# Optimization experiments

Hardware: AMD Instinct MI355X
Metric: run time of the kernel (lower is better)

The kernel has to match this reference:

```python
import jax, jax.numpy as jnp
import numpy as np

FEATURE_DIM = 1024
HIDDEN_DIM = FEATURE_DIM // 4  # MetaNet default: max(input_dim//4, output_dim) = 256
NUM_TASKS = 8
BATCH = 8192


def setup_inputs() -> dict:
    key = jax.random.key(0)
    ks = jax.random.split(key, 8)
    features = jax.random.normal(ks[0], (BATCH, FEATURE_DIM), dtype=jnp.float32)
    # meta_net: Linear(D->H) -> ReLU -> Linear(H->K). Scaled so coefficients straddle the threshold.
    W1 = jax.random.normal(ks[1], (HIDDEN_DIM, FEATURE_DIM), dtype=jnp.float32) * 0.02
    b1 = jax.random.normal(ks[2], (HIDDEN_DIM,), dtype=jnp.float32) * 0.01
    W2 = jax.random.normal(ks[3], (NUM_TASKS, HIDDEN_DIM), dtype=jnp.float32) * 0.1
    b2 = jax.random.normal(ks[4], (NUM_TASKS,), dtype=jnp.float32) * 0.05
    # per-task feature transforms, init randn * 0.01 as in the module
    task_mats = jax.random.normal(ks[5], (NUM_TASKS, FEATURE_DIM, FEATURE_DIM), dtype=jnp.float32) * 0.01
    # projection initialized to identity (nn.init.eye_)
    proj_W = jnp.eye(FEATURE_DIM, dtype=jnp.float32)
    base_threshold = jnp.array([0.05], dtype=jnp.float32)
    beta = jnp.array([1.0], dtype=jnp.float32)
    return {"features": features, "W1": W1, "b1": b1, "W2": W2, "b2": b2,
            "task_mats": task_mats, "proj_W": proj_W,
            "base_threshold": base_threshold, "beta": beta}


def reference(features, W1, b1, W2, b2, task_mats, proj_W, base_threshold, beta):
    # --- meta_net forward: coefficients [B, K] ---
    h = features @ W1.T + b1                    # [B, H]
    relu_h = jnp.maximum(h, 0.0)
    coeffs = relu_h @ W2.T + b2                 # [B, K]

    # --- gradient-based uncertainty: ||d coeff_k / d features_b||_2 ---
    # Jacobian of the 2-layer MLP: J[b,k,d] = sum_h W2[k,h] * relu'(h[b,h]) * W1[h,d]
    mask = (h > 0).astype(features.dtype)       # [B, H]
    J = jnp.einsum('kh,bh,hd->bkd', W2, mask, W1)   # [B, K, D]
    unc = jnp.sqrt(jnp.sum(J * J, axis=-1))     # [B, K]
    mx = jnp.max(unc)
    unc = jnp.where(mx > 0, unc / mx, unc)
    # torch computes this on detached features with create_graph=False -> non-differentiable
    unc = jax.lax.stop_gradient(unc)

    # --- adaptive gating ---
    base = jax.nn.softplus(base_threshold)                  # [1]
    thresholds = base * (1.0 + jax.nn.relu(beta) * unc)     # [B, K]
    gated = jnp.where(jnp.abs(coeffs) < thresholds, 0.0, coeffs)  # [B, K]

    # --- sequential weighted task-vector combination (blockwise=False) ---
    x = features                                # [B, D]
    for j in range(task_mats.shape[0]):         # small fixed K, structurally sequential
        x = x + gated[:, j:j + 1] * (x @ task_mats[j])
    return x @ proj_W.T                         # [B, D]
```

## Files before the change

### kernel.cpp

```cpp
#include <hip/hip_runtime.h>


typedef float  f32x4  __attribute__((ext_vector_type(4)));
typedef __bf16 bf16x8 __attribute__((ext_vector_type(8)));
typedef _Float16 f16x8 __attribute__((ext_vector_type(8)));
typedef _Float16 f16x4 __attribute__((ext_vector_type(4)));

__device__ __forceinline__ unsigned short f2bf(float x) {
  return __builtin_bit_cast(unsigned short, (__bf16)x);
}
__device__ __forceinline__ float bf2f(unsigned short u) {
  return (float)__builtin_bit_cast(__bf16, u);
}
__device__ __forceinline__ void ldsload16(void* lds, const void* g) {
  __builtin_amdgcn_global_load_lds(
      (const __attribute__((address_space(1))) void*)g,
      (__attribute__((address_space(3))) void*)lds, 16, 0, 0);
}


__global__ __launch_bounds__(256) void k_initsplit(const float* __restrict__ F,
                                                   _Float16* __restrict__ hi,
                                                   _Float16* __restrict__ lo,
                                                   float* __restrict__ xout,
                                                   unsigned short* __restrict__ xhA,
                                                   unsigned short* __restrict__ xhB) {
  size_t i = (size_t)blockIdx.x * 256 + threadIdx.x;
  float4 f = *(const float4*)&F[i * 4];
  _Float16 h0 = (_Float16)f.x, h1 = (_Float16)f.y, h2 = (_Float16)f.z, h3 = (_Float16)f.w;
  *(f16x4*)&hi[i * 4] = (f16x4){h0, h1, h2, h3};
  *(f16x4*)&lo[i * 4] = (f16x4){(_Float16)((f.x - (float)h0) * 2048.0f),
                                (_Float16)((f.y - (float)h1) * 2048.0f),
                                (_Float16)((f.z - (float)h2) * 2048.0f),
                                (_Float16)((f.w - (float)h3) * 2048.0f)};
  *(float4*)&xout[i * 4] = f;
  ushort4 u;
  u.x = f2bf(f.x); u.y = f2bf(f.y); u.z = f2bf(f.z); u.w = f2bf(f.w);
  *(ushort4*)&xhA[i * 4] = u;
  *(ushort4*)&xhB[i * 4] = u;
}

__global__ __launch_bounds__(256) void k_split(const float* __restrict__ src,
                                               _Float16* __restrict__ hi,
                                               _Float16* __restrict__ lo) {
  size_t i = (size_t)blockIdx.x * 256 + threadIdx.x;
  float4 f = *(const float4*)&src[i * 4];
  _Float16 h0 = (_Float16)f.x, h1 = (_Float16)f.y, h2 = (_Float16)f.z, h3 = (_Float16)f.w;
  *(f16x4*)&hi[i * 4] = (f16x4){h0, h1, h2, h3};
  *(f16x4*)&lo[i * 4] = (f16x4){(_Float16)((f.x - (float)h0) * 2048.0f),
                                (_Float16)((f.y - (float)h1) * 2048.0f),
                                (_Float16)((f.z - (float)h2) * 2048.0f),
                                (_Float16)((f.w - (float)h3) * 2048.0f)};
}

__global__ __launch_bounds__(256) void k_gram(const float* __restrict__ W1,
                                              float* __restrict__ G) {
  __shared__ float Wa[16][33], Wb[16][33];
  int t = threadIdx.x, ti = t & 15, tj = t >> 4;
  int bi = blockIdx.x, bj = blockIdx.y;
  float acc = 0.f;
  for (int kc = 0; kc < 1024; kc += 32) {
    __syncthreads();
    for (int e = t; e < 512; e += 256) {
      int r = e >> 5, k = e & 31;
      Wa[r][k] = W1[(size_t)(bi * 16 + r) * 1024 + kc + k];
      Wb[r][k] = W1[(size_t)(bj * 16 + r) * 1024 + kc + k];
    }
    __syncthreads();
#pragma unroll
    for (int k = 0; k < 32; k++) acc += Wa[ti][k] * Wb[tj][k];
  }
  G[(size_t)(bi * 16 + ti) * 256 + bj * 16 + tj] = acc;
}

__global__ __launch_bounds__(256) void k_prepA(const float* __restrict__ W2,
                                               const float* __restrict__ G,
                                               unsigned short* __restrict__ Bk,
                                               unsigned int* __restrict__ mx,
                                               int* __restrict__ cnt,
                                               int* __restrict__ cnt2,
                                               unsigned int* __restrict__ flag) {
  int k = blockIdx.x >> 8, hr = blockIdx.x & 255, t = threadIdx.x;
  if (blockIdx.x == 0) {
    if (t == 0) { *mx = 0u; *flag = 1u; }
    if (t < 8) { cnt[t] = 0; cnt2[t] = 0; }
  }
  float v = W2[k * 256 + hr] * W2[k * 256 + t] * G[(size_t)hr * 256 + t];
  float hi = bf2f(f2bf(v));
  float lo = v - hi;
  unsigned short* row = &Bk[((size_t)k * 256 + hr) * 512];
  row[t] = f2bf(hi);
  row[256 + t] = f2bf(lo);
}

__global__ __launch_bounds__(256) void k_maskcoef(const float* __restrict__ h,
                                                  const float* __restrict__ W2,
                                                  const float* __restrict__ b2,
                                                  unsigned short* __restrict__ Mb,
                                                  unsigned int* __restrict__ Mbits,
                                                  float* __restrict__ coeffs) {
  __shared__ float W2s[2048];
  __shared__ unsigned sw[4][8];
  int t = threadIdx.x;
  for (int e = t; e < 2048; e += 256) W2s[e] = W2[e];
  int w = t >> 6, l = t & 63;
  int row = blockIdx.x * 4 + w;
  float4 hv = *(const float4*)&h[(size_t)row * 256 + l * 4];
  ushort4 mv;
  mv.x = hv.x > 0.f ? 0x3F80 : 0; mv.y = hv.y > 0.f ? 0x3F80 : 0;
  mv.z = hv.z > 0.f ? 0x3F80 : 0; mv.w = hv.w > 0.f ? 0x3F80 : 0;
  *(ushort4*)&Mb[(size_t)row * 256 + l * 4] = mv;
  unsigned nib = (hv.x > 0.f ? 1u : 0u) | (hv.y > 0.f ? 2u : 0u) |
                 (hv.z > 0.f ? 4u : 0u) | (hv.w > 0.f ? 8u : 0u);
  if (l < 8) sw[w][l] = 0u;
  __syncthreads();
  atomicOr(&sw[w][l >> 3], nib << ((l & 7) * 4));
  __syncthreads();
  if (l < 8) Mbits[row * 8 + l] = sw[w][l];
  float r0 = fmaxf(hv.x, 0.f), r1 = fmaxf(hv.y, 0.f);
  float r2 = fmaxf(hv.z, 0.f), r3 = fmaxf(hv.w, 0.f);
#pragma unroll
  for (int k = 0; k < 8; k++) {
    const float* wr = &W2s[k * 256 + l * 4];
    float p = r0 * wr[0] + r1 * wr[1] + r2 * wr[2] + r3 * wr[3];
    p += __shfl_xor(p, 1);  p += __shfl_xor(p, 2);  p += __shfl_xor(p, 4);
    p += __shfl_xor(p, 8);  p += __shfl_xor(p, 16); p += __shfl_xor(p, 32);
    if (l == 0) coeffs[row * 8 + k] = p + b2[k];
  }
}

__global__ __launch_bounds__(256) void k_max(const float* __restrict__ unc2,
                                             unsigned int* __restrict__ mx) {
  int i = blockIdx.x * 256 + threadIdx.x;
  float v = 0.f;
  for (; i < 65536; i += 64 * 256) v = fmaxf(v, unc2[i]);
#pragma unroll
  for (int d = 1; d < 64; d <<= 1) v = fmaxf(v, __shfl_xor(v, d));
  __shared__ float sm[4];
  if ((threadIdx.x & 63) == 0) sm[threadIdx.x >> 6] = v;
  __syncthreads();
  if (threadIdx.x == 0) {
    v = fmaxf(fmaxf(sm[0], sm[1]), fmaxf(sm[2], sm[3]));
    atomicMax(mx, __float_as_uint(v));
  }
}

__global__ __launch_bounds__(256) void k_gateidx(const float* __restrict__ coeffs,
                                                 const float* __restrict__ unc2,
                                                 const unsigned int* __restrict__ mxb,
                                                 const float* __restrict__ btp,
                                                 const float* __restrict__ betap,
                                                 unsigned short* __restrict__ rowidx,
                                                 float* __restrict__ gcomp,
                                                 int* __restrict__ cnt,
                                                 unsigned short* __restrict__ rowidx2,
                                                 int* __restrict__ cnt2) {
  __shared__ int lc[8], base[8], lc2[8], base2[8];
  __shared__ float sgv[256];
  int t = threadIdx.x;
  if (t < 8) { lc[t] = 0; lc2[t] = 0; }
  __syncthreads();
  int i = blockIdx.x * 256 + t;
  float c = coeffs[i];
  float u2 = fmaxf(unc2[i], 0.f);
  float un = sqrtf(u2);
  float m = sqrtf(__uint_as_float(*mxb));
  float u = (m > 0.f) ? un / m : un;
  float base_t = (float)log1p(exp((double)btp[0]));
  float br = fmaxf(betap[0], 0.f);
  float thr = base_t * (1.0f + br * u);
  float gv = (fabsf(c) < thr) ? 0.f : c;
  sgv[t] = gv;
  int jj = i & 7, row = i >> 3, slot = -1;
  if (gv != 0.f) slot = atomicAdd(&lc[jj], 1);
  __syncthreads();
  int slot2 = -1;
  if (jj >= 1 && gv == 0.f && sgv[t - 1] != 0.f) slot2 = atomicAdd(&lc2[jj], 1);
  __syncthreads();
  if (t < 8) {
    base[t]  = lc[t]  ? atomicAdd(&cnt[t],  lc[t])  : 0;
    base2[t] = lc2[t] ? atomicAdd(&cnt2[t], lc2[t]) : 0;
  }
  __syncthreads();
  if (slot >= 0) {
    int pos = base[jj] + slot;
    rowidx[jj * 8192 + pos] = (unsigned short)row;
    gcomp[jj * 8192 + pos] = gv;
  }
  if (slot2 >= 0)
    rowidx2[jj * 8192 + base2[jj] + slot2] = (unsigned short)row;
}

__global__ __launch_bounds__(256) void k_prepT(const float* __restrict__ TM,
                                               unsigned short* __restrict__ Tb) {
  __shared__ float Ls[64][65];
  int bid = blockIdx.x;
  int jj = bid >> 8, kt = (bid >> 4) & 15, nt = bid & 15;
  int t = threadIdx.x;
  int r = t >> 2, c0 = (t & 3) * 16;
  const float* src = TM + (size_t)jj * 1048576 + (size_t)(kt * 64 + r) * 1024 + nt * 64 + c0;
  float4 v0 = *(const float4*)&src[0];
  float4 v1 = *(const float4*)&src[4];
  float4 v2 = *(const float4*)&src[8];
  float4 v3 = *(const float4*)&src[12];
  float tmp[16] = {v0.x, v0.y, v0.z, v0.w, v1.x, v1.y, v1.z, v1.w,
                   v2.x, v2.y, v2.z, v2.w, v3.x, v3.y, v3.z, v3.w};
#pragma unroll
  for (int i = 0; i < 16; i++) Ls[r][c0 + i] = tmp[i];
  __syncthreads();
  int nr = t >> 2, kc = (t & 3) * 16;
  union { unsigned short s[16]; uint4 v[2]; } p;
#pragma unroll
  for (int i = 0; i < 16; i++) p.s[i] = f2bf(Ls[kc + i][nr]);
  unsigned short* dst = Tb + (size_t)jj * 1048576 + (size_t)(nt * 64 + nr) * 1024 + kt * 64 + kc;
  *(uint4*)&dst[0] = p.v[0];
  *(uint4*)&dst[8] = p.v[1];
}

__global__ __launch_bounds__(256) void k_prepP2(const float* __restrict__ P,
                                                unsigned short* __restrict__ Pb,
                                                unsigned int* __restrict__ flag) {
  size_t i = (size_t)blockIdx.x * 256 + threadIdx.x;
  float4 f = *(const float4*)&P[i * 4];
  ushort4 u;
  u.x = f2bf(f.x); u.y = f2bf(f.y); u.z = f2bf(f.z); u.w = f2bf(f.w);
  *(ushort4*)&Pb[i * 4] = u;
  size_t e = i * 4;
  bool bad = false;
#pragma unroll
  for (int s = 0; s < 4; s++) {
    size_t ee = e + s;
    float exp = ((ee >> 10) == (ee & 1023)) ? 1.0f : 0.0f;
    float got = (s == 0) ? f.x : (s == 1) ? f.y : (s == 2) ? f.z : f.w;
    if (got != exp) bad = true;
  }
  if (bad) atomicAnd(flag, 0u);
}


__global__ __launch_bounds__(256) void k_gemm_h2(const _Float16* __restrict__ Fhi,
                                                 const _Float16* __restrict__ Flo,
                                                 const _Float16* __restrict__ W1h,
                                                 const _Float16* __restrict__ W1l,
                                                 const float* __restrict__ b1,
                                                 float* __restrict__ hout) {
  __shared__ __attribute__((aligned(16))) _Float16 Ah[64 * 32];
  __shared__ __attribute__((aligned(16))) _Float16 Al[64 * 32];
  __shared__ __attribute__((aligned(16))) _Float16 Bh[64 * 32];
  __shared__ __attribute__((aligned(16))) _Float16 Bl[64 * 32];
  int t = threadIdx.x, w = t >> 6, l = t & 63, q = l >> 4, li = l & 15;
  int wm = w >> 1, wn = w & 1;
  int ib = blockIdx.x, jb = blockIdx.y;
  f32x4 acc0[2][2] = {}, acc1[2][2] = {};
  int srow = t >> 2, sg = (((t & 3) - (srow >> 1)) & 3) * 8;
  for (int k0 = 0; k0 < 1024; k0 += 32) {
    __syncthreads();
    size_t ao = (size_t)(ib * 64 + srow) * 1024 + k0 + sg;
    size_t bo = (size_t)(jb * 64 + srow) * 1024 + k0 + sg;
    ldsload16((void*)(Ah + (w * 64) * 8), Fhi + ao);
    ldsload16((void*)(Al + (w * 64) * 8), Flo + ao);
    ldsload16((void*)(Bh + (w * 64) * 8), W1h + bo);
    ldsload16((void*)(Bl + (w * 64) * 8), W1l + bo);
    __syncthreads();
    f16x8 ah[2], al[2], bh[2], bl[2];
#pragma unroll
    for (int mt = 0; mt < 2; mt++) {
      int r = wm * 32 + mt * 16 + li;
      int c = ((q + (r >> 1)) & 3) * 8;
      ah[mt] = *(const f16x8*)&Ah[r * 32 + c];
      al[mt] = *(const f16x8*)&Al[r * 32 + c];
    }
#pragma unroll
    for (int nt = 0; nt < 2; nt++) {
      int rr = wn * 32 + nt * 16 + li;
      int c = ((q + (rr >> 1)) & 3) * 8;
      bh[nt] = *(const f16x8*)&Bh[rr * 32 + c];
      bl[nt] = *(const f16x8*)&Bl[rr * 32 + c];
    }
#pragma unroll
    for (int mt = 0; mt < 2; mt++)
#pragma unroll
      for (int nt = 0; nt < 2; nt++) {
        acc0[mt][nt] = __builtin_amdgcn_mfma_f32_16x16x32_f16(ah[mt], bh[nt], acc0[mt][nt], 0, 0, 0);
        acc1[mt][nt] = __builtin_amdgcn_mfma_f32_16x16x32_f16(ah[mt], bl[nt], acc1[mt][nt], 0, 0, 0);
        acc1[mt][nt] = __builtin_amdgcn_mfma_f32_16x16x32_f16(al[mt], bh[nt], acc1[mt][nt], 0, 0, 0);
      }
  }
  const float sc = 1.0f / 2048.0f;
#pragma unroll
  for (int mt = 0; mt < 2; mt++) {
    int grow = ib * 64 + wm * 32 + mt * 16 + q * 4;
#pragma unroll
    for (int nt = 0; nt < 2; nt++) {
      int gcol = jb * 64 + wn * 32 + nt * 16 + li;
      float bb = b1[gcol];
#pragma unroll
      for (int r = 0; r < 4; r++)
        hout[(size_t)(grow + r) * 256 + gcol] = acc0[mt][nt][r] + acc1[mt][nt][r] * sc + bb;
    }
  }
}

__global__ __launch_bounds__(512) void k_gemm_unc2(const unsigned short* __restrict__ Mb,
                                                   const unsigned short* __restrict__ BkAll,
                                                   const unsigned int* __restrict__ Mbits,
                                                   float* __restrict__ unc2) {
  __shared__ __attribute__((aligned(16))) unsigned short As[128 * 32];
  __shared__ __attribute__((aligned(16))) unsigned short Bs[256 * 32];
  __shared__ float Red[128][4];
  int t = threadIdx.x, w = t >> 6, l = t & 63, q = l >> 4, li = l & 15;
  int wm = w >> 2, wn = w & 3;
  int rb = blockIdx.x, kidx = blockIdx.y;
  const unsigned short* Bk = BkAll + (size_t)kidx * 256 * 512;
  f32x4 acc[4][4] = {};
  for (int k0 = 0; k0 < 512; k0 += 32) {
    __syncthreads();
    {
      int row = t >> 2, g = (((t & 3) - (row >> 1)) & 3) * 8;
      ldsload16((void*)(As + (size_t)(w * 64) * 8),
                Mb + (size_t)(rb * 128 + row) * 256 + (k0 & 255) + g);
    }
#pragma unroll
    for (int i = 0; i < 2; i++) {
      int idx = i * 512 + t, row = idx >> 2, g = (((idx & 3) - (row >> 1)) & 3) * 8;
      ldsload16((void*)(Bs + (size_t)(i * 512 + w * 64) * 8),
                Bk + (size_t)row * 512 + k0 + g);
    }
    __syncthreads();
    bf16x8 av[4], bv[4];
#pragma unroll
    for (int mt = 0; mt < 4; mt++) {
      int r = wm * 64 + mt * 16 + li;
      av[mt] = *(const bf16x8*)&As[r * 32 + ((q + (r >> 1)) & 3) * 8];
    }
#pragma unroll
    for (int nt = 0; nt < 4; nt++) {
      int rc = wn * 64 + nt * 16 + li;
      bv[nt] = *(const bf16x8*)&Bs[rc * 32 + ((q + (rc >> 1)) & 3) * 8];
    }
#pragma unroll
    for (int mt = 0; mt < 4; mt++)
#pragma unroll
      for (int nt = 0; nt < 4; nt++)
        acc[mt][nt] = __builtin_amdgcn_mfma_f32_16x16x32_bf16(av[mt], bv[nt], acc[mt][nt], 0, 0, 0);
  }
#pragma unroll
  for (int mt = 0; mt < 4; mt++) {
#pragma unroll
    for (int r = 0; r < 4; r++) {
      int rl = wm * 64 + mt * 16 + q * 4 + r;
      int grow = rb * 128 + rl;
      unsigned m0 = Mbits[(size_t)grow * 8 + wn * 2];
      unsigned m1 = Mbits[(size_t)grow * 8 + wn * 2 + 1];
      float p = 0.f;
#pragma unroll
      for (int nt = 0; nt < 4; nt++) {
        unsigned mword = (nt < 2) ? m0 : m1;
        int sh = (nt & 1) * 16 + li;
        if ((mword >> sh) & 1u) p += acc[mt][nt][r];
      }
      p += __shfl_xor(p, 1); p += __shfl_xor(p, 2);
      p += __shfl_xor(p, 4); p += __shfl_xor(p, 8);
      if (li == 0) Red[rl][wn] = p;
    }
  }
  __syncthreads();
  if (t < 128)
    unc2[(size_t)(rb * 128 + t) * 8 + kidx] =
        Red[t][0] + Red[t][1] + Red[t][2] + Red[t][3];
}

__global__ __launch_bounds__(1024) void k_chain8(const unsigned short* __restrict__ cur,
                                                 unsigned short* __restrict__ nxt,
                                                 const unsigned short* __restrict__ Tb,
                                                 const unsigned short* __restrict__ rowidx,
                                                 const int* __restrict__ cnt,
                                                 const unsigned short* __restrict__ rowidx2,
                                                 const int* __restrict__ cnt2,
                                                 const float* __restrict__ gcomp,
                                                 float* __restrict__ xout, int j) {
  int Mj = min(max(cnt[j], 0), 8192);
  __shared__ __attribute__((aligned(16))) unsigned short As[64 * 512];
  __shared__ __attribute__((aligned(16))) unsigned short Bs[64 * 512];
  int t = threadIdx.x, w = t >> 6, l = t & 63, q = l >> 4, li = l & 15;
  int wm = w >> 2, wn = w & 3;
  int bx = blockIdx.x, jb = blockIdx.y;
  int bid = jb * 16 + bx;
  const unsigned short* ridx = rowidx + j * 8192;
  {
    int M2 = min(max(cnt2[j], 0), 8192);
    for (int cm2 = bid; cm2 < M2; cm2 += 256) {
      int row = rowidx2[j * 8192 + cm2] & 8191;
      if (t < 128)
        *(uint4*)&nxt[(size_t)row * 1024 + t * 8] =
            *(const uint4*)&cur[(size_t)row * 1024 + t * 8];
    }
  }
  for (int ib = bx; ib * 64 < Mj; ib += 16) {
    f32x4 acc = {};
#pragma unroll 1
    for (int half = 0; half < 2; half++) {
      __syncthreads();
#pragma unroll
      for (int i = 0; i < 4; i++) {
        int slot = i * 1024 + t;
        int r = slot >> 6, kcs = slot & 63;
        int kcg = kcs ^ (r & 7);
        int cm = ib * 64 + r;
        int grow = ridx[cm < Mj ? cm : Mj - 1] & 8191;
        ldsload16((void*)(As + (size_t)(i * 1024 + w * 64) * 8),
                  cur + (size_t)grow * 1024 + half * 512 + kcg * 8);
      }
#pragma unroll
      for (int i = 0; i < 4; i++) {
        int slot = i * 1024 + t;
        int n = slot >> 6, kcs = slot & 63;
        int kcg = kcs ^ (n & 7);
        ldsload16((void*)(Bs + (size_t)(i * 1024 + w * 64) * 8),
                  Tb + (size_t)(jb * 64 + n) * 1024 + half * 512 + kcg * 8);
      }
      __syncthreads();
#pragma unroll
      for (int s = 0; s < 16; s++) {
        int r = wm * 16 + li;
        bf16x8 av = *(const bf16x8*)&As[((size_t)r * 64 + ((s * 4 + q) ^ (r & 7))) * 8];
        int n = wn * 16 + li;
        bf16x8 bv = *(const bf16x8*)&Bs[((size_t)n * 64 + ((s * 4 + q) ^ (n & 7))) * 8];
        acc = __builtin_amdgcn_mfma_f32_16x16x32_bf16(av, bv, acc, 0, 0, 0);
      }
    }
#pragma unroll
    for (int r = 0; r < 4; r++) {
      int cm = ib * 64 + wm * 16 + q * 4 + r;
      if (cm >= Mj) continue;
      int grow = ridx[cm] & 8191;
      float g = gcomp[j * 8192 + cm];
      size_t off = (size_t)grow * 1024 + jb * 64 + wn * 16 + li;
      float xv = fmaf(g, acc[r], xout[off]);
      xout[off] = xv;
      nxt[off] = f2bf(xv);
    }
  }
}

__global__ __launch_bounds__(256) void k_proj3(const unsigned short* __restrict__ xcur,
                                               const unsigned short* __restrict__ Pb,
                                               float* __restrict__ out,
                                               const unsigned int* __restrict__ flag) {
  if (*flag) return;
  __shared__ __attribute__((aligned(16))) unsigned short As[128 * 32];
  __shared__ __attribute__((aligned(16))) unsigned short Bs[128 * 32];
  int t = threadIdx.x, w = t >> 6, l = t & 63, q = l >> 4, li = l & 15;
  int wm = w >> 1, wn = w & 1;
  int ib = blockIdx.x, jb = blockIdx.y;
  f32x4 acc[4][4] = {};
  for (int k0 = 0; k0 < 1024; k0 += 32) {
    __syncthreads();
    const unsigned short* ga = xcur + (size_t)(ib * 128) * 1024 + k0;
    const unsigned short* gb = Pb + (size_t)(jb * 128) * 1024 + k0;
#pragma unroll
    for (int i = 0; i < 2; i++) {
      int idx = i * 256 + t, row = idx >> 2, kc = (idx & 3) * 8;
      ldsload16((void*)(As + (i * 256 + w * 64) * 8), ga + (size_t)row * 1024 + kc);
      ldsload16((void*)(Bs + (i * 256 + w * 64) * 8), gb + (size_t)row * 1024 + kc);
    }
    __syncthreads();
    bf16x8 av[4], bv[4];
#pragma unroll
    for (int mt = 0; mt < 4; mt++)
      av[mt] = *(const bf16x8*)&As[(wm * 64 + mt * 16 + li) * 32 + q * 8];
#pragma unroll
    for (int nt = 0; nt < 4; nt++)
      bv[nt] = *(const bf16x8*)&Bs[(wn * 64 + nt * 16 + li) * 32 + q * 8];
#pragma unroll
    for (int mt = 0; mt < 4; mt++)
#pragma unroll
      for (int nt = 0; nt < 4; nt++)
        acc[mt][nt] = __builtin_amdgcn_mfma_f32_16x16x32_bf16(av[mt], bv[nt], acc[mt][nt], 0, 0, 0);
  }
#pragma unroll
  for (int mt = 0; mt < 4; mt++) {
    int grow = ib * 128 + wm * 64 + mt * 16 + q * 4;
#pragma unroll
    for (int nt = 0; nt < 4; nt++) {
      int gcol = jb * 128 + wn * 64 + nt * 16 + li;
#pragma unroll
      for (int r = 0; r < 4; r++)
        out[(size_t)(grow + r) * 1024 + gcol] = acc[mt][nt][r];
    }
  }
}


extern "C" void kernel_launch(void* const* d_in, const int* in_sizes, int n_in,
                              void* d_out, int out_size, void* d_ws, size_t ws_size,
                              hipStream_t stream) {
  const float* F    = (const float*)d_in[0];
  const float* W1   = (const float*)d_in[1];
  const float* b1   = (const float*)d_in[2];
  const float* W2   = (const float*)d_in[3];
  const float* b2   = (const float*)d_in[4];
  const float* TM   = (const float*)d_in[5];
  const float* PW   = (const float*)d_in[6];
  const float* bt   = (const float*)d_in[7];
  const float* beta = (const float*)d_in[8];

  char* w = (char*)d_ws;
  float*          hbuf   = (float*)         (w + 0);
  unsigned short* Mb     = (unsigned short*)(w + 8388608);
  unsigned int*   Mbits  = (unsigned int*)  (w + 12582912);
  float*          coeffs = (float*)         (w + 12845056);
  float*          unc2   = (float*)         (w + 13107200);
  float*          G      = (float*)         (w + 13369344);
  unsigned short* Bk     = (unsigned short*)(w + 13631488);
  _Float16*       W1h    = (_Float16*)      (w + 15728640);
  _Float16*       W1l    = (_Float16*)      (w + 16252928);
  unsigned short* Tb     = (unsigned short*)(w + 0);
  char*           buf0   =                  (w + 16777216);
  char*           buf1   =                  (w + 33554432);
  unsigned int*   mx     = (unsigned int*)  (w + 50331648);
  int*            cnt    = (int*)           (w + 50331652);
  int*            cnt2   = (int*)           (w + 50331684);
  unsigned int*   flag   = (unsigned int*)  (w + 50331716);
  unsigned short* rowidx = (unsigned short*)(w + 50332160);
  unsigned short* rowidx2= (unsigned short*)(w + 50463232);
  float*          gcomp  = (float*)         (w + 50594304);
  unsigned short* xhA    = (unsigned short*)(w + 50856448);
  unsigned short* xhB    = (unsigned short*)(w + 67633664);
  float* xout = (float*)d_out;

  k_initsplit<<<8192, 256, 0, stream>>>(F, (_Float16*)buf0, (_Float16*)buf1, xout, xhA, xhB);
  k_split<<<256, 256, 0, stream>>>(W1, W1h, W1l);
  k_gram<<<dim3(16, 16), 256, 0, stream>>>(W1, G);
  k_gemm_h2<<<dim3(128, 4), 256, 0, stream>>>((const _Float16*)buf0, (const _Float16*)buf1,
                                              W1h, W1l, b1, hbuf);
  k_maskcoef<<<2048, 256, 0, stream>>>(hbuf, W2, b2, Mb, Mbits, coeffs);
  k_prepA<<<2048, 256, 0, stream>>>(W2, G, Bk, mx, cnt, cnt2, flag);
  k_gemm_unc2<<<dim3(64, 8), 512, 0, stream>>>(Mb, Bk, Mbits, unc2);
  k_max<<<64, 256, 0, stream>>>(unc2, mx);
  k_gateidx<<<256, 256, 0, stream>>>(coeffs, unc2, mx, bt, beta,
                                     rowidx, gcomp, cnt, rowidx2, cnt2);

  k_prepT<<<2048, 256, 0, stream>>>(TM, Tb);
  for (int j = 0; j < 8; j++) {
    const unsigned short* cur = (j & 1) ? xhB : xhA;
    unsigned short*       nxt = (j & 1) ? xhA : xhB;
    k_chain8<<<dim3(16, 16), 1024, 0, stream>>>(cur, nxt, Tb + (size_t)j * 1048576,
                                                rowidx, cnt, rowidx2, cnt2,
                                                gcomp, xout, j);
  }

  unsigned short* Pb = (unsigned short*)buf1;
  k_prepP2<<<1024, 256, 0, stream>>>(PW, Pb, flag);
  k_proj3<<<dim3(64, 8), 256, 0, stream>>>(xhA, Pb, xout, flag);
}
```

Baseline: 352.8 us.

## Fuse prep kernels, split features inside GEMM, and fold max into uncertainty GEMM

Drops the separate fp16 hi/lo split of the feature matrix. The h GEMM now loads fp32 features into LDS through an XOR-swizzled layout and splits them into hi/lo in registers. W1 split and Gram computation merge into one launch, and the projection conversion merges with the task-matrix prep. The max reduction moves into the uncertainty GEMM epilogue via atomicMax, removing several launches and the 64 MB of hi/lo feature traffic, at the cost of extra conversion ALU work and twice the LDS load bytes per GEMM tile.

```diff
diff --git a/kernel.cpp b/kernel.cpp
--- a/kernel.cpp
+++ b/kernel.cpp
@@ -19,20 +19,12 @@
 }
 
 
-__global__ __launch_bounds__(256) void k_initsplit(const float* __restrict__ F,
-                                                   _Float16* __restrict__ hi,
-                                                   _Float16* __restrict__ lo,
-                                                   float* __restrict__ xout,
-                                                   unsigned short* __restrict__ xhA,
-                                                   unsigned short* __restrict__ xhB) {
+__global__ __launch_bounds__(256) void k_initsplit2(const float* __restrict__ F,
+                                                    float* __restrict__ xout,
+                                                    unsigned short* __restrict__ xhA,
+                                                    unsigned short* __restrict__ xhB) {
   size_t i = (size_t)blockIdx.x * 256 + threadIdx.x;
   float4 f = *(const float4*)&F[i * 4];
-  _Float16 h0 = (_Float16)f.x, h1 = (_Float16)f.y, h2 = (_Float16)f.z, h3 = (_Float16)f.w;
-  *(f16x4*)&hi[i * 4] = (f16x4){h0, h1, h2, h3};
-  *(f16x4*)&lo[i * 4] = (f16x4){(_Float16)((f.x - (float)h0) * 2048.0f),
-                                (_Float16)((f.y - (float)h1) * 2048.0f),
-                                (_Float16)((f.z - (float)h2) * 2048.0f),
-                                (_Float16)((f.w - (float)h3) * 2048.0f)};
   *(float4*)&xout[i * 4] = f;
   ushort4 u;
   u.x = f2bf(f.x); u.y = f2bf(f.y); u.z = f2bf(f.z); u.w = f2bf(f.w);
@@ -40,24 +32,26 @@
   *(ushort4*)&xhB[i * 4] = u;
 }
 
-__global__ __launch_bounds__(256) void k_split(const float* __restrict__ src,
+__global__ __launch_bounds__(256) void k_prep1(const float* __restrict__ W1,
                                                _Float16* __restrict__ hi,
-                                               _Float16* __restrict__ lo) {
-  size_t i = (size_t)blockIdx.x * 256 + threadIdx.x;
-  float4 f = *(const float4*)&src[i * 4];
-  _Float16 h0 = (_Float16)f.x, h1 = (_Float16)f.y, h2 = (_Float16)f.z, h3 = (_Float16)f.w;
-  *(f16x4*)&hi[i * 4] = (f16x4){h0, h1, h2, h3};
-  *(f16x4*)&lo[i * 4] = (f16x4){(_Float16)((f.x - (float)h0) * 2048.0f),
-                                (_Float16)((f.y - (float)h1) * 2048.0f),
-                                (_Float16)((f.z - (float)h2) * 2048.0f),
-                                (_Float16)((f.w - (float)h3) * 2048.0f)};
-}
-
-__global__ __launch_bounds__(256) void k_gram(const float* __restrict__ W1,
-                                              float* __restrict__ G) {
+                                               _Float16* __restrict__ lo,
+                                               float* __restrict__ G) {
   __shared__ float Wa[16][33], Wb[16][33];
-  int t = threadIdx.x, ti = t & 15, tj = t >> 4;
-  int bi = blockIdx.x, bj = blockIdx.y;
+  int t = threadIdx.x;
+  if (blockIdx.x < 256) {
+    size_t i = (size_t)blockIdx.x * 256 + t;
+    float4 f = *(const float4*)&W1[i * 4];
+    _Float16 h0 = (_Float16)f.x, h1 = (_Float16)f.y, h2 = (_Float16)f.z, h3 = (_Float16)f.w;
+    *(f16x4*)&hi[i * 4] = (f16x4){h0, h1, h2, h3};
+    *(f16x4*)&lo[i * 4] = (f16x4){(_Float16)((f.x - (float)h0) * 2048.0f),
+                                  (_Float16)((f.y - (float)h1) * 2048.0f),
+                                  (_Float16)((f.z - (float)h2) * 2048.0f),
+                                  (_Float16)((f.w - (float)h3) * 2048.0f)};
+    return;
+  }
+  int bid2 = blockIdx.x - 256;
+  int bi = bid2 & 15, bj = bid2 >> 4;
+  int ti = t & 15, tj = t >> 4;
   float acc = 0.f;
   for (int kc = 0; kc < 1024; kc += 32) {
     __syncthreads();
@@ -129,22 +123,6 @@
   }
 }
 
-__global__ __launch_bounds__(256) void k_max(const float* __restrict__ unc2,
-                                             unsigned int* __restrict__ mx) {
-  int i = blockIdx.x * 256 + threadIdx.x;
-  float v = 0.f;
-  for (; i < 65536; i += 64 * 256) v = fmaxf(v, unc2[i]);
-#pragma unroll
-  for (int d = 1; d < 64; d <<= 1) v = fmaxf(v, __shfl_xor(v, d));
-  __shared__ float sm[4];
-  if ((threadIdx.x & 63) == 0) sm[threadIdx.x >> 6] = v;
-  __syncthreads();
-  if (threadIdx.x == 0) {
-    v = fmaxf(fmaxf(sm[0], sm[1]), fmaxf(sm[2], sm[3]));
-    atomicMax(mx, __float_as_uint(v));
-  }
-}
-
 __global__ __launch_bounds__(256) void k_gateidx(const float* __restrict__ coeffs,
                                                  const float* __restrict__ unc2,
                                                  const unsigned int* __restrict__ mxb,
@@ -191,12 +169,33 @@
     rowidx2[jj * 8192 + base2[jj] + slot2] = (unsigned short)row;
 }
 
-__global__ __launch_bounds__(256) void k_prepT(const float* __restrict__ TM,
-                                               unsigned short* __restrict__ Tb) {
+__global__ __launch_bounds__(256) void k_prepTP(const float* __restrict__ TM,
+                                                unsigned short* __restrict__ Tb,
+                                                const float* __restrict__ P,
+                                                unsigned short* __restrict__ Pb,
+                                                unsigned int* __restrict__ flag) {
   __shared__ float Ls[64][65];
   int bid = blockIdx.x;
+  int t = threadIdx.x;
+  if (bid >= 2048) {
+    size_t i = (size_t)(bid - 2048) * 256 + t;
+    float4 f = *(const float4*)&P[i * 4];
+    ushort4 u;
+    u.x = f2bf(f.x); u.y = f2bf(f.y); u.z = f2bf(f.z); u.w = f2bf(f.w);
+    *(ushort4*)&Pb[i * 4] = u;
+    size_t e = i * 4;
+    bool bad = false;
+#pragma unroll
+    for (int s = 0; s < 4; s++) {
+      size_t ee = e + s;
+      float exp = ((ee >> 10) == (ee & 1023)) ? 1.0f : 0.0f;
+      float got = (s == 0) ? f.x : (s == 1) ? f.y : (s == 2) ? f.z : f.w;
+      if (got != exp) bad = true;
+    }
+    if (bad) atomicAnd(flag, 0u);
+    return;
+  }
   int jj = bid >> 8, kt = (bid >> 4) & 15, nt = bid & 15;
-  int t = threadIdx.x;
   int r = t >> 2, c0 = (t & 3) * 16;
   const float* src = TM + (size_t)jj * 1048576 + (size_t)(kt * 64 + r) * 1024 + nt * 64 + c0;
   float4 v0 = *(const float4*)&src[0];
@@ -217,58 +216,50 @@
   *(uint4*)&dst[8] = p.v[1];
 }
 
-__global__ __launch_bounds__(256) void k_prepP2(const float* __restrict__ P,
-                                                unsigned short* __restrict__ Pb,
-                                                unsigned int* __restrict__ flag) {
-  size_t i = (size_t)blockIdx.x * 256 + threadIdx.x;
-  float4 f = *(const float4*)&P[i * 4];
-  ushort4 u;
-  u.x = f2bf(f.x); u.y = f2bf(f.y); u.z = f2bf(f.z); u.w = f2bf(f.w);
-  *(ushort4*)&Pb[i * 4] = u;
-  size_t e = i * 4;
-  bool bad = false;
-#pragma unroll
-  for (int s = 0; s < 4; s++) {
-    size_t ee = e + s;
-    float exp = ((ee >> 10) == (ee & 1023)) ? 1.0f : 0.0f;
-    float got = (s == 0) ? f.x : (s == 1) ? f.y : (s == 2) ? f.z : f.w;
-    if (got != exp) bad = true;
-  }
-  if (bad) atomicAnd(flag, 0u);
-}
-
-
-__global__ __launch_bounds__(256) void k_gemm_h2(const _Float16* __restrict__ Fhi,
-                                                 const _Float16* __restrict__ Flo,
+
+__global__ __launch_bounds__(256) void k_gemm_h3(const float* __restrict__ F,
                                                  const _Float16* __restrict__ W1h,
                                                  const _Float16* __restrict__ W1l,
                                                  const float* __restrict__ b1,
                                                  float* __restrict__ hout) {
-  __shared__ __attribute__((aligned(16))) _Float16 Ah[64 * 32];
-  __shared__ __attribute__((aligned(16))) _Float16 Al[64 * 32];
+  __shared__ __attribute__((aligned(16))) float    Af[64 * 32];
   __shared__ __attribute__((aligned(16))) _Float16 Bh[64 * 32];
   __shared__ __attribute__((aligned(16))) _Float16 Bl[64 * 32];
   int t = threadIdx.x, w = t >> 6, l = t & 63, q = l >> 4, li = l & 15;
   int wm = w >> 1, wn = w & 1;
   int ib = blockIdx.x, jb = blockIdx.y;
   f32x4 acc0[2][2] = {}, acc1[2][2] = {};
-  int srow = t >> 2, sg = (((t & 3) - (srow >> 1)) & 3) * 8;
+  int brow = t >> 2, bg = (((t & 3) - (brow >> 1)) & 3) * 8;
   for (int k0 = 0; k0 < 1024; k0 += 32) {
     __syncthreads();
-    size_t ao = (size_t)(ib * 64 + srow) * 1024 + k0 + sg;
-    size_t bo = (size_t)(jb * 64 + srow) * 1024 + k0 + sg;
-    ldsload16((void*)(Ah + (w * 64) * 8), Fhi + ao);
-    ldsload16((void*)(Al + (w * 64) * 8), Flo + ao);
-    ldsload16((void*)(Bh + (w * 64) * 8), W1h + bo);
-    ldsload16((void*)(Bl + (w * 64) * 8), W1l + bo);
+#pragma unroll
+    for (int i = 0; i < 2; i++) {
+      int slot = i * 256 + t, r = slot >> 3, c = slot & 7;
+      int g = c ^ (r & 7);
+      ldsload16((void*)(Af + (size_t)(i * 256 + w * 64) * 4),
+                F + (size_t)(ib * 64 + r) * 1024 + k0 + g * 4);
+    }
+    {
+      size_t bo = (size_t)(jb * 64 + brow) * 1024 + k0 + bg;
+      ldsload16((void*)(Bh + (w * 64) * 8), W1h + bo);
+      ldsload16((void*)(Bl + (w * 64) * 8), W1l + bo);
+    }
     __syncthreads();
     f16x8 ah[2], al[2], bh[2], bl[2];
 #pragma unroll
     for (int mt = 0; mt < 2; mt++) {
       int r = wm * 32 + mt * 16 + li;
-      int c = ((q + (r >> 1)) & 3) * 8;
-      ah[mt] = *(const f16x8*)&Ah[r * 32 + c];
-      al[mt] = *(const f16x8*)&Al[r * 32 + c];
+      f32x4 a0 = *(const f32x4*)&Af[r * 32 + ((2 * q) ^ (r & 7)) * 4];
+      f32x4 a1 = *(const f32x4*)&Af[r * 32 + ((2 * q + 1) ^ (r & 7)) * 4];
+#pragma unroll
+      for (int jx = 0; jx < 4; jx++) {
+        _Float16 h0 = (_Float16)a0[jx];
+        ah[mt][jx] = h0;
+        al[mt][jx] = (_Float16)((a0[jx] - (float)h0) * 2048.0f);
+        _Float16 h1 = (_Float16)a1[jx];
+        ah[mt][4 + jx] = h1;
+        al[mt][4 + jx] = (_Float16)((a1[jx] - (float)h1) * 2048.0f);
+      }
     }
 #pragma unroll
     for (int nt = 0; nt < 2; nt++) {
@@ -304,7 +295,8 @@
 __global__ __launch_bounds__(512) void k_gemm_unc2(const unsigned short* __restrict__ Mb,
                                                    const unsigned short* __restrict__ BkAll,
                                                    const unsigned int* __restrict__ Mbits,
-                                                   float* __restrict__ unc2) {
+                                                   float* __restrict__ unc2,
+                                                   unsigned int* __restrict__ mx) {
   __shared__ __attribute__((aligned(16))) unsigned short As[128 * 32];
   __shared__ __attribute__((aligned(16))) unsigned short Bs[256 * 32];
   __shared__ float Red[128][4];
@@ -365,9 +357,14 @@
     }
   }
   __syncthreads();
-  if (t < 128)
-    unc2[(size_t)(rb * 128 + t) * 8 + kidx] =
-        Red[t][0] + Red[t][1] + Red[t][2] + Red[t][3];
+  if (t < 128) {
+    float s = Red[t][0] + Red[t][1] + Red[t][2] + Red[t][3];
+    unc2[(size_t)(rb * 128 + t) * 8 + kidx] = s;
+    float v = fmaxf(s, 0.f);
+#pragma unroll
+    for (int d = 1; d < 64; d <<= 1) v = fmaxf(v, __shfl_xor(v, d));
+    if ((t & 63) == 0) atomicMax(mx, __float_as_uint(v));
+  }
 }
 
 __global__ __launch_bounds__(1024) void k_chain8(const unsigned short* __restrict__ cur,
@@ -516,7 +513,6 @@
   _Float16*       W1h    = (_Float16*)      (w + 15728640);
   _Float16*       W1l    = (_Float16*)      (w + 16252928);
   unsigned short* Tb     = (unsigned short*)(w + 0);
-  char*           buf0   =                  (w + 16777216);
   char*           buf1   =                  (w + 33554432);
   unsigned int*   mx     = (unsigned int*)  (w + 50331648);
   int*            cnt    = (int*)           (w + 50331652);
@@ -529,19 +525,17 @@
   unsigned short* xhB    = (unsigned short*)(w + 67633664);
   float* xout = (float*)d_out;
 
-  k_initsplit<<<8192, 256, 0, stream>>>(F, (_Float16*)buf0, (_Float16*)buf1, xout, xhA, xhB);
-  k_split<<<256, 256, 0, stream>>>(W1, W1h, W1l);
-  k_gram<<<dim3(16, 16), 256, 0, stream>>>(W1, G);
-  k_gemm_h2<<<dim3(128, 4), 256, 0, stream>>>((const _Float16*)buf0, (const _Float16*)buf1,
-                                              W1h, W1l, b1, hbuf);
+  k_initsplit2<<<8192, 256, 0, stream>>>(F, xout, xhA, xhB);
+  k_prep1<<<512, 256, 0, stream>>>(W1, W1h, W1l, G);
+  k_gemm_h3<<<dim3(128, 4), 256, 0, stream>>>(F, W1h, W1l, b1, hbuf);
   k_maskcoef<<<2048, 256, 0, stream>>>(hbuf, W2, b2, Mb, Mbits, coeffs);
   k_prepA<<<2048, 256, 0, stream>>>(W2, G, Bk, mx, cnt, cnt2, flag);
-  k_gemm_unc2<<<dim3(64, 8), 512, 0, stream>>>(Mb, Bk, Mbits, unc2);
-  k_max<<<64, 256, 0, stream>>>(unc2, mx);
+  k_gemm_unc2<<<dim3(64, 8), 512, 0, stream>>>(Mb, Bk, Mbits, unc2, mx);
   k_gateidx<<<256, 256, 0, stream>>>(coeffs, unc2, mx, bt, beta,
                                      rowidx, gcomp, cnt, rowidx2, cnt2);
 
-  k_prepT<<<2048, 256, 0, stream>>>(TM, Tb);
+  unsigned short* Pb = (unsigned short*)buf1;
+  k_prepTP<<<3072, 256, 0, stream>>>(TM, Tb, PW, Pb, flag);
   for (int j = 0; j < 8; j++) {
     const unsigned short* cur = (j & 1) ? xhB : xhA;
     unsigned short*       nxt = (j & 1) ? xhA : xhB;
@@ -550,7 +544,5 @@
                                                 gcomp, xout, j);
   }
 
-  unsigned short* Pb = (unsigned short*)buf1;
-  k_prepP2<<<1024, 256, 0, stream>>>(PW, Pb, flag);
   k_proj3<<<dim3(64, 8), 256, 0, stream>>>(xhA, Pb, xout, flag);
 }
```

New measurement: 354.4 us. Within noise of the previous version (+0.4%).
